# Kernel tuning notes

Hardware: AMD Instinct MI355X
Metric: run time of the kernel (lower is better)

The kernel has to match this reference:

```python
import jax, jax.numpy as jnp
import numpy as np

N_NODES = 50000
N_EDGES = 800000
EMB = 128
NODE_F = 128
EDGE_F = 16
L = 5
BN_EPS = 1e-5


def setup_inputs() -> dict:
    key = jax.random.key(0)
    ks = jax.random.split(key, 12)
    inp = {
        "x": jax.random.normal(ks[0], (N_NODES, NODE_F), jnp.float32),
        "edge_attr": jax.random.normal(ks[1], (N_EDGES, EDGE_F), jnp.float32),
        "edge_index": jax.random.randint(ks[2], (2, N_EDGES), 0, N_NODES, jnp.int32),
        "Wx": jax.random.normal(ks[3], (NODE_F, EMB), jnp.float32) / np.sqrt(NODE_F),
        "bx": jax.random.normal(ks[4], (EMB,), jnp.float32) * 0.01,
        "We": jax.random.normal(ks[5], (L, EDGE_F, EMB), jnp.float32) / np.sqrt(EDGE_F),
        "be": jax.random.normal(ks[6], (L, EMB), jnp.float32) * 0.01,
        "W1": jax.random.normal(ks[7], (L, EMB, 2 * EMB), jnp.float32) / np.sqrt(EMB),
        "b1": jax.random.normal(ks[8], (L, 2 * EMB), jnp.float32) * 0.01,
        "W2": jax.random.normal(ks[9], (L, 2 * EMB, EMB), jnp.float32) / np.sqrt(2 * EMB),
        "b2": jax.random.normal(ks[10], (L, EMB), jnp.float32) * 0.01,
        "gamma": jnp.ones((L, EMB), jnp.float32),
        "beta": jnp.zeros((L, EMB), jnp.float32),
    }
    return inp


def reference(x, edge_attr, edge_index, Wx, bx, We, be, W1, b1, W2, b2, gamma, beta):
    n = x.shape[0]
    num_layers = We.shape[0]
    # add self loops with zero edge attributes (bias of edge_embedding still applies)
    self_idx = jnp.arange(n, dtype=edge_index.dtype)
    src = jnp.concatenate([edge_index[0], self_idx])
    dst = jnp.concatenate([edge_index[1], self_idx])
    ea = jnp.concatenate([edge_attr, jnp.zeros((n, edge_attr.shape[1]), edge_attr.dtype)], axis=0)

    h = x @ Wx + bx  # x_embedding0: [N, EMB]
    for l in range(num_layers):
        eemb = ea @ We[l] + be[l]                     # [E+N, EMB]
        msg = h[src] + eemb                            # gather + add
        agg = jax.ops.segment_sum(msg, dst, num_segments=n)  # scatter-add
        # GIN MLP: emb -> 2*emb -> emb
        h2 = jax.nn.relu(agg @ W1[l] + b1[l]) @ W2[l] + b2[l]
        # BatchNorm1d (training mode: batch statistics, biased variance)
        mean = jnp.mean(h2, axis=0)
        var = jnp.mean((h2 - mean) ** 2, axis=0)
        h2 = (h2 - mean) * jax.lax.rsqrt(var + BN_EPS) * gamma[l] + beta[l]
        if l < num_layers - 1:
            h2 = jax.nn.relu(h2)
        # dropout with drop_ratio=0 is identity
        h = h2
    return h  # JK == 'last'
```

## Files before the change

### kernel.cpp

```cpp
#include <hip/hip_runtime.h>

typedef __bf16 bf16;
typedef __bf16 bf16x2 __attribute__((ext_vector_type(2)));
typedef __bf16 bf16x4 __attribute__((ext_vector_type(4)));
typedef __bf16 bf16x8 __attribute__((ext_vector_type(8)));
typedef float f32x4 __attribute__((ext_vector_type(4)));

#define NN 50000
#define NE 800000
#define EMB 128
#define EDGE_F 16
#define NLAYER 5
#define SCAN_BLOCKS 196

__global__ __launch_bounds__(256) void swz_kernel(
    const float* __restrict__ Wx, const float* __restrict__ W1,
    const float* __restrict__ W2, const float* __restrict__ We,
    bf16* __restrict__ wx_s, bf16* __restrict__ w1_s,
    bf16* __restrict__ w2_s, float* __restrict__ weT)
{
    int t = blockIdx.x * 256 + threadIdx.x;
    if (t < 16384) {
        int k = t >> 7, n = t & 127;
        wx_s[(((k >> 5) << 7) + n) * 32 + (k & 31)] = (bf16)Wx[t];
    } else if (t < 16384 + 163840) {
        int u = t - 16384;
        int l = u / 32768, r = u % 32768;
        int k = r >> 8, n = r & 255;
        w1_s[l * 32768 + (((k >> 5) << 8) + n) * 32 + (k & 31)] = (bf16)W1[u];
    } else if (t < 16384 + 327680) {
        int u = t - (16384 + 163840);
        int l = u / 32768, r = u % 32768;
        int k = r >> 7, n = r & 127;
        w2_s[l * 32768 + (((k >> 5) << 7) + n) * 32 + (k & 31)] = (bf16)W2[u];
    } else if (t < 16384 + 327680 + 10240) {
        int u = t - (16384 + 327680);
        int l = u >> 11, r = u & 2047;
        int c = r >> 4, f = r & 15;
        weT[u] = We[l * 2048 + f * 128 + c];
    }
}

__global__ void count_kernel(const int* __restrict__ dst, int* __restrict__ deg, int nE)
{
    int e = blockIdx.x * 256 + threadIdx.x;
    if (e < nE) atomicAdd(&deg[dst[e]], 1);
}

__global__ __launch_bounds__(256) void deg_bsum_kernel(
    const int* __restrict__ deg, int* __restrict__ bsum, int n)
{
    __shared__ int red[256];
    int i = blockIdx.x * 256 + threadIdx.x;
    red[threadIdx.x] = (i < n) ? deg[i] : 0;
    __syncthreads();
    for (int s = 128; s > 0; s >>= 1) {
        if (threadIdx.x < s) red[threadIdx.x] += red[threadIdx.x + s];
        __syncthreads();
    }
    if (threadIdx.x == 0) bsum[blockIdx.x] = red[0];
}

__global__ __launch_bounds__(256) void bsum_scan_kernel(
    const int* __restrict__ bsum, int* __restrict__ boff,
    int* __restrict__ rowstart, int nb, int n)
{
    __shared__ int v[256];
    int t = threadIdx.x;
    v[t] = (t < nb) ? bsum[t] : 0;
    __syncthreads();
    if (t == 0) {
        int r = 0;
        for (int i = 0; i < nb; ++i) { int x = v[i]; v[i] = r; r += x; }
        rowstart[n] = r;
    }
    __syncthreads();
    if (t < nb) boff[t] = v[t];
}

__global__ __launch_bounds__(256) void chunk_scan_kernel(
    const int* __restrict__ deg, const int* __restrict__ boff,
    int* __restrict__ rowstart, int* __restrict__ cursor, int n)
{
    __shared__ int v[256];
    int t = threadIdx.x;
    int i = blockIdx.x * 256 + t;
    int x = (i < n) ? deg[i] : 0;
    v[t] = x;
    __syncthreads();
    for (int s = 1; s < 256; s <<= 1) {
        int add = (t >= s) ? v[t - s] : 0;
        __syncthreads();
        v[t] += add;
        __syncthreads();
    }
    int ex = v[t] - x + boff[blockIdx.x];
    if (i < n) { rowstart[i] = ex; cursor[i] = ex; }
}

__global__ void fill_kernel(const int* __restrict__ src, const int* __restrict__ dst,
                            int* __restrict__ cursor, int* __restrict__ csr_src,
                            int* __restrict__ csr_e, int nE)
{
    int e = blockIdx.x * 256 + threadIdx.x;
    if (e < nE) {
        int d = dst[e];
        int pos = atomicAdd(&cursor[d], 1);
        csr_src[pos] = src[e];
        csr_e[pos] = e;
    }
}

__global__ __launch_bounds__(256) void ea_gather_kernel(
    const float* __restrict__ edge_attr, const int* __restrict__ rowstart,
    const int* __restrict__ csr_e, float* __restrict__ ea_agg, int n)
{
    int node = blockIdx.x * 16 + (threadIdx.x >> 4);
    int f = threadIdx.x & 15;
    if (node >= n) return;
    int rs = rowstart[node], re = rowstart[node + 1];
    float a = 0.f;
    for (int j = rs; j < re; ++j) {
        int e = csr_e[j];
        a += edge_attr[(size_t)e * EDGE_F + f];
    }
    ea_agg[node * EDGE_F + f] = a;
}

__global__ __launch_bounds__(256) void agg_kernel(
    const bf16* __restrict__ h, const int* __restrict__ rowstart,
    const int* __restrict__ csr_src, const float* __restrict__ ea_agg,
    const float* __restrict__ weT_l, const float* __restrict__ be_l,
    bf16* __restrict__ agg, int n)
{
    int lane = threadIdx.x & 63;
    int node = blockIdx.x * 4 + (threadIdx.x >> 6);
    if (node >= n) return;
    int rs = rowstart[node], re = rowstart[node + 1];
    int c0 = lane * 2;
    float ax = 0.f, ay = 0.f;
    bf16x2 hself = *(const bf16x2*)(h + (size_t)node * EMB + c0);
    int j = rs;
    for (; j + 8 <= re; j += 8) {
        int s0 = csr_src[j], s1 = csr_src[j + 1], s2 = csr_src[j + 2], s3 = csr_src[j + 3];
        int s4 = csr_src[j + 4], s5 = csr_src[j + 5], s6 = csr_src[j + 6], s7 = csr_src[j + 7];
        bf16x2 h0 = *(const bf16x2*)(h + (size_t)s0 * EMB + c0);
        bf16x2 h1 = *(const bf16x2*)(h + (size_t)s1 * EMB + c0);
        bf16x2 h2v = *(const bf16x2*)(h + (size_t)s2 * EMB + c0);
        bf16x2 h3 = *(const bf16x2*)(h + (size_t)s3 * EMB + c0);
        bf16x2 h4 = *(const bf16x2*)(h + (size_t)s4 * EMB + c0);
        bf16x2 h5 = *(const bf16x2*)(h + (size_t)s5 * EMB + c0);
        bf16x2 h6 = *(const bf16x2*)(h + (size_t)s6 * EMB + c0);
        bf16x2 h7 = *(const bf16x2*)(h + (size_t)s7 * EMB + c0);
        ax += (float)h0.x + (float)h1.x + (float)h2v.x + (float)h3.x
            + (float)h4.x + (float)h5.x + (float)h6.x + (float)h7.x;
        ay += (float)h0.y + (float)h1.y + (float)h2v.y + (float)h3.y
            + (float)h4.y + (float)h5.y + (float)h6.y + (float)h7.y;
    }
    for (; j < re; ++j) {
        int s = csr_src[j];
        bf16x2 hv = *(const bf16x2*)(h + (size_t)s * EMB + c0);
        ax += (float)hv.x; ay += (float)hv.y;
    }
    ax += (float)hself.x; ay += (float)hself.y;
    {
        const float* ea = ea_agg + node * EDGE_F;
        const float* w0 = weT_l + (size_t)c0 * 16;
        const float* w1 = weT_l + (size_t)(c0 + 1) * 16;
#pragma unroll
        for (int f = 0; f < 16; ++f) {
            float ef = ea[f];
            ax += ef * w0[f];
            ay += ef * w1[f];
        }
    }
    {
        float dp1 = (float)(re - rs + 1);
        ax += dp1 * be_l[c0];
        ay += dp1 * be_l[c0 + 1];
    }
    bf16x2 o; o.x = (bf16)ax; o.y = (bf16)ay;
    *(bf16x2*)(agg + (size_t)node * EMB + c0) = o;
}

template <int K, int N, bool RELU, bool AFP32, bool STATS>
__global__ __launch_bounds__(256) void gemm_kernel(
    const void* __restrict__ Ap, const bf16* __restrict__ Bswz,
    const float* __restrict__ bias, bf16* __restrict__ outp,
    float* __restrict__ psum, int M)
{
    __shared__ float lstat[STATS ? 1024 : 1];
    if constexpr (STATS) {
        for (int i = threadIdx.x; i < 1024; i += 256) lstat[i] = 0.f;
        __syncthreads();
    }
    const int lane = threadIdx.x & 63;
    const int wave = threadIdx.x >> 6;
    const int m0 = (blockIdx.x * 4 + wave) * 16;
    if (m0 >= M) return;
    const int m = lane & 15, q = lane >> 4;
    constexpr int NF = N / 16, KB = K / 32;

    f32x4 acc[NF];
#pragma unroll
    for (int f = 0; f < NF; ++f) acc[f] = 0.f;

#pragma unroll
    for (int kb = 0; kb < KB; ++kb) {
        bf16x8 a;
        if constexpr (AFP32) {
            const float* ar = (const float*)Ap + (size_t)(m0 + m) * K + kb * 32 + q * 8;
            f32x4 v0 = *(const f32x4*)ar;
            f32x4 v1 = *(const f32x4*)(ar + 4);
#pragma unroll
            for (int j = 0; j < 4; ++j) { a[j] = (bf16)v0[j]; a[4 + j] = (bf16)v1[j]; }
        } else {
            const bf16* ar = (const bf16*)Ap + (size_t)(m0 + m) * K + kb * 32 + q * 8;
            a = *(const bf16x8*)ar;
        }
#pragma unroll
        for (int f = 0; f < NF; ++f) {
            bf16x8 b = *(const bf16x8*)(Bswz + ((size_t)(kb * N + f * 16 + m)) * 32 + q * 8);
            acc[f] = __builtin_amdgcn_mfma_f32_16x16x32_bf16(a, b, acc[f], 0, 0, 0);
        }
    }

#pragma unroll
    for (int f = 0; f < NF; ++f) {
        const int col = f * 16 + m;
        float bv = bias[col];
        float s1 = 0.f, s2 = 0.f;
#pragma unroll
        for (int r = 0; r < 4; ++r) {
            float v = acc[f][r] + bv;
            if (RELU) v = fmaxf(v, 0.f);
            int row = m0 + q * 4 + r;
            outp[(size_t)row * N + col] = (bf16)v;
            if constexpr (STATS) { s1 += v; s2 += v * v; }
        }
        if constexpr (STATS) {
            s1 += __shfl_xor(s1, 16); s1 += __shfl_xor(s1, 32);
            s2 += __shfl_xor(s2, 16); s2 += __shfl_xor(s2, 32);
            if (q == 0) {
                lstat[wave * 128 + col] = s1;
                lstat[512 + wave * 128 + col] = s2;
            }
        }
    }
    if constexpr (STATS) {
        __syncthreads();
        int t = threadIdx.x;
        if (t < 128) {
            float s = lstat[t] + lstat[128 + t] + lstat[256 + t] + lstat[384 + t];
            float ssq = lstat[512 + t] + lstat[640 + t] + lstat[768 + t] + lstat[896 + t];
            psum[(size_t)blockIdx.x * 256 + t] = s;
            psum[(size_t)blockIdx.x * 256 + 128 + t] = ssq;
        }
    }
}

__global__ __launch_bounds__(256) void reduce_stats_kernel(
    const float* __restrict__ psum, float* __restrict__ stats, int nblk)
{
    int c = threadIdx.x;
    float acc = 0.f;
    for (int b = blockIdx.x; b < nblk; b += gridDim.x)
        acc += psum[(size_t)b * 256 + c];
    atomicAdd(&stats[c], acc);
}

__global__ __launch_bounds__(256) void norm_kernel(
    const bf16* __restrict__ h2, const float* __restrict__ sums,
    const float* __restrict__ sumsq, const float* __restrict__ gamma,
    const float* __restrict__ beta, void* __restrict__ outp, int n,
    int relu, int out_fp32)
{
    __shared__ float sc[EMB], sh[EMB];
    int tid = threadIdx.x;
    if (tid < EMB) {
        float inv_n = 1.0f / (float)n;
        float mean = sums[tid] * inv_n;
        float var = sumsq[tid] * inv_n - mean * mean;
        float s = gamma[tid] * rsqrtf(var + 1e-5f);
        sc[tid] = s;
        sh[tid] = beta[tid] - mean * s;
    }
    __syncthreads();
    int total4 = n * (EMB / 4);
    int stride = gridDim.x * blockDim.x;
    for (int i = blockIdx.x * blockDim.x + tid; i < total4; i += stride) {
        bf16x4 hv = ((const bf16x4*)h2)[i];
        int c0 = (i * 4) & (EMB - 1);
        float v0 = (float)hv.x * sc[c0] + sh[c0];
        float v1 = (float)hv.y * sc[c0 + 1] + sh[c0 + 1];
        float v2 = (float)hv.z * sc[c0 + 2] + sh[c0 + 2];
        float v3 = (float)hv.w * sc[c0 + 3] + sh[c0 + 3];
        if (relu) {
            v0 = fmaxf(v0, 0.f); v1 = fmaxf(v1, 0.f);
            v2 = fmaxf(v2, 0.f); v3 = fmaxf(v3, 0.f);
        }
        if (out_fp32) {
            f32x4 o; o.x = v0; o.y = v1; o.z = v2; o.w = v3;
            ((f32x4*)outp)[i] = o;
        } else {
            bf16x4 o;
            o.x = (bf16)v0; o.y = (bf16)v1; o.z = (bf16)v2; o.w = (bf16)v3;
            ((bf16x4*)outp)[i] = o;
        }
    }
}

extern "C" void kernel_launch(void* const* d_in, const int* in_sizes, int n_in,
                              void* d_out, int out_size, void* d_ws, size_t ws_size,
                              hipStream_t stream)
{
    const float* x         = (const float*)d_in[0];
    const float* edge_attr = (const float*)d_in[1];
    const int*   eidx      = (const int*)d_in[2];
    const float* Wx        = (const float*)d_in[3];
    const float* bx        = (const float*)d_in[4];
    const float* We        = (const float*)d_in[5];
    const float* be        = (const float*)d_in[6];
    const float* W1        = (const float*)d_in[7];
    const float* b1        = (const float*)d_in[8];
    const float* W2        = (const float*)d_in[9];
    const float* b2        = (const float*)d_in[10];
    const float* gamma     = (const float*)d_in[11];
    const float* beta      = (const float*)d_in[12];

    size_t off = 0;
    char* base = (char*)d_ws;
    auto alloc = [&](size_t bytes) -> void* {
        void* p = base + off;
        off += (bytes + 255) & ~(size_t)255;
        return p;
    };
    int*   deg      = (int*)alloc(NN * 4);
    float* stats    = (float*)alloc(NLAYER * 256 * 4);
    size_t zero_bytes = off;
    int*   rowstart = (int*)alloc((NN + 1) * 4);
    int*   cursor   = (int*)alloc(NN * 4);
    int*   bsum     = (int*)alloc(SCAN_BLOCKS * 4);
    int*   boff     = (int*)alloc(SCAN_BLOCKS * 4);
    int*   csr_src  = (int*)alloc((size_t)NE * 4);
    int*   csr_e    = (int*)alloc((size_t)NE * 4);
    float* ea_agg   = (float*)alloc((size_t)NN * EDGE_F * 4);
    bf16*  h        = (bf16*)alloc((size_t)NN * EMB * 2);
    bf16*  aggb     = (bf16*)alloc((size_t)NN * EMB * 2);
    bf16*  t1       = (bf16*)alloc((size_t)NN * 2 * EMB * 2);
    bf16*  h2b      = (bf16*)alloc((size_t)NN * EMB * 2);
    float* psum     = (float*)alloc((size_t)782 * 256 * 4);
    bf16*  wx_s     = (bf16*)alloc(16384 * 2);
    bf16*  w1_s     = (bf16*)alloc(163840 * 2);
    bf16*  w2_s     = (bf16*)alloc(163840 * 2);
    float* weT      = (float*)alloc(10240 * 4);
    (void)ws_size; (void)in_sizes; (void)n_in; (void)out_size;

    const int* src = eidx;
    const int* dst = eidx + NE;

    hipMemsetAsync(d_ws, 0, zero_bytes, stream);

    swz_kernel<<<1384, 256, 0, stream>>>(Wx, W1, W2, We, wx_s, w1_s, w2_s, weT);
    count_kernel<<<NE / 256, 256, 0, stream>>>(dst, deg, NE);
    deg_bsum_kernel<<<SCAN_BLOCKS, 256, 0, stream>>>(deg, bsum, NN);
    bsum_scan_kernel<<<1, 256, 0, stream>>>(bsum, boff, rowstart, SCAN_BLOCKS, NN);
    chunk_scan_kernel<<<SCAN_BLOCKS, 256, 0, stream>>>(deg, boff, rowstart, cursor, NN);
    fill_kernel<<<NE / 256, 256, 0, stream>>>(src, dst, cursor, csr_src, csr_e, NE);
    ea_gather_kernel<<<NN / 16, 256, 0, stream>>>(edge_attr, rowstart, csr_e, ea_agg, NN);

    const int gemm_blocks = (NN / 16 + 3) / 4;
    gemm_kernel<128, 128, false, true, false><<<gemm_blocks, 256, 0, stream>>>(
        x, wx_s, bx, h, nullptr, NN);

    for (int l = 0; l < NLAYER; ++l) {
        float* stats_l = stats + l * 256;
        agg_kernel<<<NN / 4, 256, 0, stream>>>(
            h, rowstart, csr_src, ea_agg, weT + l * 2048, be + l * EMB, aggb, NN);
        gemm_kernel<128, 256, true, false, false><<<gemm_blocks, 256, 0, stream>>>(
            aggb, w1_s + l * 32768, b1 + l * 2 * EMB, t1, nullptr, NN);
        gemm_kernel<256, 128, false, false, true><<<gemm_blocks, 256, 0, stream>>>(
            t1, w2_s + l * 32768, b2 + l * EMB, h2b, psum, NN);
        reduce_stats_kernel<<<8, 256, 0, stream>>>(psum, stats_l, gemm_blocks);
        norm_kernel<<<1024, 256, 0, stream>>>(
            h2b, stats_l, stats_l + 128, gamma + l * EMB, beta + l * EMB,
            (l == NLAYER - 1) ? d_out : (void*)h, NN,
            (l < NLAYER - 1) ? 1 : 0, (l == NLAYER - 1) ? 1 : 0);
    }
}
```

Before: 1.030 ms.

## Store node features in column-sliced layout for cache-friendly aggregation gathers

Node features, aggregates and GEMM outputs are stored in 8 column slices of 16 channels ([slice][node][16]). The aggregation kernel processes one slice per block, so each gather touches only a 32-byte row segment and a slice's working set (~1.6 MB) can stay in cache. The edge-embedding term is moved into a separate eaw_kernel that writes a precomputed bf16 tensor each layer. This adds an extra pass over a full N×128 buffer per layer and more kernel launches, and the GEMMs and the norm kernel need index math adapted to the sliced layout.

```diff
diff --git a/kernel.cpp b/kernel.cpp
--- a/kernel.cpp
+++ b/kernel.cpp
@@ -15,9 +15,8 @@
 
 __global__ __launch_bounds__(256) void swz_kernel(
     const float* __restrict__ Wx, const float* __restrict__ W1,
-    const float* __restrict__ W2, const float* __restrict__ We,
-    bf16* __restrict__ wx_s, bf16* __restrict__ w1_s,
-    bf16* __restrict__ w2_s, float* __restrict__ weT)
+    const float* __restrict__ W2,
+    bf16* __restrict__ wx_s, bf16* __restrict__ w1_s, bf16* __restrict__ w2_s)
 {
     int t = blockIdx.x * 256 + threadIdx.x;
     if (t < 16384) {
@@ -33,11 +32,6 @@
         int l = u / 32768, r = u % 32768;
         int k = r >> 7, n = r & 127;
         w2_s[l * 32768 + (((k >> 5) << 7) + n) * 32 + (k & 31)] = (bf16)W2[u];
-    } else if (t < 16384 + 327680 + 10240) {
-        int u = t - (16384 + 327680);
-        int l = u >> 11, r = u & 2047;
-        int c = r >> 4, f = r & 15;
-        weT[u] = We[l * 2048 + f * 128 + c];
     }
 }
 
@@ -127,63 +121,74 @@
     ea_agg[node * EDGE_F + f] = a;
 }
 
+__global__ __launch_bounds__(256) void eaw_kernel(
+    const float* __restrict__ ea_agg, const int* __restrict__ rowstart,
+    const float* __restrict__ We_l, const float* __restrict__ be_l,
+    bf16* __restrict__ eawb, int n)
+{
+    int i = blockIdx.x * 256 + threadIdx.x;
+    int o = i * 2;
+    if (o >= n * EMB) return;
+    int slice = o / (n * 16);
+    int r = o - slice * (n * 16);
+    int node = r >> 4;
+    int c0 = slice * 16 + (r & 15);
+    float dp1 = (float)(rowstart[node + 1] - rowstart[node] + 1);
+    const float* ea = ea_agg + (size_t)node * EDGE_F;
+    float v0 = dp1 * be_l[c0], v1 = dp1 * be_l[c0 + 1];
+#pragma unroll
+    for (int f = 0; f < 16; ++f) {
+        float e = ea[f];
+        v0 += e * We_l[f * EMB + c0];
+        v1 += e * We_l[f * EMB + c0 + 1];
+    }
+    bf16x2 ov; ov.x = (bf16)v0; ov.y = (bf16)v1;
+    *(bf16x2*)(eawb + o) = ov;
+}
+
 __global__ __launch_bounds__(256) void agg_kernel(
-    const bf16* __restrict__ h, const int* __restrict__ rowstart,
-    const int* __restrict__ csr_src, const float* __restrict__ ea_agg,
-    const float* __restrict__ weT_l, const float* __restrict__ be_l,
-    bf16* __restrict__ agg, int n)
-{
-    int lane = threadIdx.x & 63;
-    int node = blockIdx.x * 4 + (threadIdx.x >> 6);
+    const bf16* __restrict__ hsm, const int* __restrict__ rowstart,
+    const int* __restrict__ csr_src, const bf16* __restrict__ eawb,
+    bf16* __restrict__ aggb, int n)
+{
+    const int tid = threadIdx.x;
+    const int slice = blockIdx.x & 7;
+    const int chunk = blockIdx.x >> 3;
+    const int node = chunk * 32 + (tid >> 3);
+    const int ql = tid & 7;
     if (node >= n) return;
-    int rs = rowstart[node], re = rowstart[node + 1];
-    int c0 = lane * 2;
-    float ax = 0.f, ay = 0.f;
-    bf16x2 hself = *(const bf16x2*)(h + (size_t)node * EMB + c0);
+    const size_t sbase = (size_t)slice * n * 16;
+    const bf16* hs = hsm + sbase + ql * 2;
+    const int rs = rowstart[node], re = rowstart[node + 1];
+    float a0 = 0.f, a1 = 0.f;
     int j = rs;
-    for (; j + 8 <= re; j += 8) {
+    for (; j + 4 <= re; j += 4) {
         int s0 = csr_src[j], s1 = csr_src[j + 1], s2 = csr_src[j + 2], s3 = csr_src[j + 3];
-        int s4 = csr_src[j + 4], s5 = csr_src[j + 5], s6 = csr_src[j + 6], s7 = csr_src[j + 7];
-        bf16x2 h0 = *(const bf16x2*)(h + (size_t)s0 * EMB + c0);
-        bf16x2 h1 = *(const bf16x2*)(h + (size_t)s1 * EMB + c0);
-        bf16x2 h2v = *(const bf16x2*)(h + (size_t)s2 * EMB + c0);
-        bf16x2 h3 = *(const bf16x2*)(h + (size_t)s3 * EMB + c0);
-        bf16x2 h4 = *(const bf16x2*)(h + (size_t)s4 * EMB + c0);
-        bf16x2 h5 = *(const bf16x2*)(h + (size_t)s5 * EMB + c0);
-        bf16x2 h6 = *(const bf16x2*)(h + (size_t)s6 * EMB + c0);
-        bf16x2 h7 = *(const bf16x2*)(h + (size_t)s7 * EMB + c0);
-        ax += (float)h0.x + (float)h1.x + (float)h2v.x + (float)h3.x
-            + (float)h4.x + (float)h5.x + (float)h6.x + (float)h7.x;
-        ay += (float)h0.y + (float)h1.y + (float)h2v.y + (float)h3.y
-            + (float)h4.y + (float)h5.y + (float)h6.y + (float)h7.y;
+        bf16x2 r0 = *(const bf16x2*)(hs + (size_t)s0 * 16);
+        bf16x2 r1 = *(const bf16x2*)(hs + (size_t)s1 * 16);
+        bf16x2 r2 = *(const bf16x2*)(hs + (size_t)s2 * 16);
+        bf16x2 r3 = *(const bf16x2*)(hs + (size_t)s3 * 16);
+        a0 += ((float)r0.x + (float)r1.x) + ((float)r2.x + (float)r3.x);
+        a1 += ((float)r0.y + (float)r1.y) + ((float)r2.y + (float)r3.y);
     }
     for (; j < re; ++j) {
         int s = csr_src[j];
-        bf16x2 hv = *(const bf16x2*)(h + (size_t)s * EMB + c0);
-        ax += (float)hv.x; ay += (float)hv.y;
-    }
-    ax += (float)hself.x; ay += (float)hself.y;
+        bf16x2 rv = *(const bf16x2*)(hs + (size_t)s * 16);
+        a0 += (float)rv.x; a1 += (float)rv.y;
+    }
     {
-        const float* ea = ea_agg + node * EDGE_F;
-        const float* w0 = weT_l + (size_t)c0 * 16;
-        const float* w1 = weT_l + (size_t)(c0 + 1) * 16;
-#pragma unroll
-        for (int f = 0; f < 16; ++f) {
-            float ef = ea[f];
-            ax += ef * w0[f];
-            ay += ef * w1[f];
-        }
+        bf16x2 rv = *(const bf16x2*)(hs + (size_t)node * 16);
+        a0 += (float)rv.x; a1 += (float)rv.y;
     }
     {
-        float dp1 = (float)(re - rs + 1);
-        ax += dp1 * be_l[c0];
-        ay += dp1 * be_l[c0 + 1];
-    }
-    bf16x2 o; o.x = (bf16)ax; o.y = (bf16)ay;
-    *(bf16x2*)(agg + (size_t)node * EMB + c0) = o;
-}
-
-template <int K, int N, bool RELU, bool AFP32, bool STATS>
+        bf16x2 ev = *(const bf16x2*)(eawb + sbase + (size_t)node * 16 + ql * 2);
+        a0 += (float)ev.x; a1 += (float)ev.y;
+    }
+    bf16x2 o; o.x = (bf16)a0; o.y = (bf16)a1;
+    *(bf16x2*)(aggb + sbase + (size_t)node * 16 + ql * 2) = o;
+}
+
+template <int K, int N, bool RELU, bool AFP32, bool STATS, bool ASM, bool OSM>
 __global__ __launch_bounds__(256) void gemm_kernel(
     const void* __restrict__ Ap, const bf16* __restrict__ Bswz,
     const float* __restrict__ bias, bf16* __restrict__ outp,
@@ -214,6 +219,10 @@
             f32x4 v1 = *(const f32x4*)(ar + 4);
 #pragma unroll
             for (int j = 0; j < 4; ++j) { a[j] = (bf16)v0[j]; a[4 + j] = (bf16)v1[j]; }
+        } else if constexpr (ASM) {
+            const bf16* ar = (const bf16*)Ap
+                + ((size_t)(kb * 2 + (q >> 1)) * M + (m0 + m)) * 16 + (q & 1) * 8;
+            a = *(const bf16x8*)ar;
         } else {
             const bf16* ar = (const bf16*)Ap + (size_t)(m0 + m) * K + kb * 32 + q * 8;
             a = *(const bf16x8*)ar;
@@ -235,7 +244,10 @@
             float v = acc[f][r] + bv;
             if (RELU) v = fmaxf(v, 0.f);
             int row = m0 + q * 4 + r;
-            outp[(size_t)row * N + col] = (bf16)v;
+            if constexpr (OSM)
+                outp[((size_t)f * M + row) * 16 + m] = (bf16)v;
+            else
+                outp[(size_t)row * N + col] = (bf16)v;
             if constexpr (STATS) { s1 += v; s2 += v * v; }
         }
         if constexpr (STATS) {
@@ -273,7 +285,7 @@
     const bf16* __restrict__ h2, const float* __restrict__ sums,
     const float* __restrict__ sumsq, const float* __restrict__ gamma,
     const float* __restrict__ beta, void* __restrict__ outp, int n,
-    int relu, int out_fp32)
+    int relu, int out_fp32, int sm)
 {
     __shared__ float sc[EMB], sh[EMB];
     int tid = threadIdx.x;
@@ -290,7 +302,14 @@
     int stride = gridDim.x * blockDim.x;
     for (int i = blockIdx.x * blockDim.x + tid; i < total4; i += stride) {
         bf16x4 hv = ((const bf16x4*)h2)[i];
-        int c0 = (i * 4) & (EMB - 1);
+        int c0;
+        if (sm) {
+            int o = i * 4;
+            int slice = o / (n * 16);
+            c0 = slice * 16 + ((o - slice * (n * 16)) & 15);
+        } else {
+            c0 = (i * 4) & (EMB - 1);
+        }
         float v0 = (float)hv.x * sc[c0] + sh[c0];
         float v1 = (float)hv.y * sc[c0 + 1] + sh[c0 + 1];
         float v2 = (float)hv.z * sc[c0 + 2] + sh[c0 + 2];
@@ -347,13 +366,13 @@
     float* ea_agg   = (float*)alloc((size_t)NN * EDGE_F * 4);
     bf16*  h        = (bf16*)alloc((size_t)NN * EMB * 2);
     bf16*  aggb     = (bf16*)alloc((size_t)NN * EMB * 2);
+    bf16*  eawb     = (bf16*)alloc((size_t)NN * EMB * 2);
     bf16*  t1       = (bf16*)alloc((size_t)NN * 2 * EMB * 2);
     bf16*  h2b      = (bf16*)alloc((size_t)NN * EMB * 2);
     float* psum     = (float*)alloc((size_t)782 * 256 * 4);
     bf16*  wx_s     = (bf16*)alloc(16384 * 2);
     bf16*  w1_s     = (bf16*)alloc(163840 * 2);
     bf16*  w2_s     = (bf16*)alloc(163840 * 2);
-    float* weT      = (float*)alloc(10240 * 4);
     (void)ws_size; (void)in_sizes; (void)n_in; (void)out_size;
 
     const int* src = eidx;
@@ -361,7 +380,7 @@
 
     hipMemsetAsync(d_ws, 0, zero_bytes, stream);
 
-    swz_kernel<<<1384, 256, 0, stream>>>(Wx, W1, W2, We, wx_s, w1_s, w2_s, weT);
+    swz_kernel<<<1344, 256, 0, stream>>>(Wx, W1, W2, wx_s, w1_s, w2_s);
     count_kernel<<<NE / 256, 256, 0, stream>>>(dst, deg, NE);
     deg_bsum_kernel<<<SCAN_BLOCKS, 256, 0, stream>>>(deg, bsum, NN);
     bsum_scan_kernel<<<1, 256, 0, stream>>>(bsum, boff, rowstart, SCAN_BLOCKS, NN);
@@ -370,21 +389,29 @@
     ea_gather_kernel<<<NN / 16, 256, 0, stream>>>(edge_attr, rowstart, csr_e, ea_agg, NN);
 
     const int gemm_blocks = (NN / 16 + 3) / 4;
-    gemm_kernel<128, 128, false, true, false><<<gemm_blocks, 256, 0, stream>>>(
+    gemm_kernel<128, 128, false, true, false, false, true><<<gemm_blocks, 256, 0, stream>>>(
         x, wx_s, bx, h, nullptr, NN);
 
+    const int agg_blocks = ((NN + 31) / 32) * 8;
     for (int l = 0; l < NLAYER; ++l) {
         float* stats_l = stats + l * 256;
-        agg_kernel<<<NN / 4, 256, 0, stream>>>(
-            h, rowstart, csr_src, ea_agg, weT + l * 2048, be + l * EMB, aggb, NN);
-        gemm_kernel<128, 256, true, false, false><<<gemm_blocks, 256, 0, stream>>>(
+        eaw_kernel<<<(NN * EMB / 2) / 256, 256, 0, stream>>>(
+            ea_agg, rowstart, We + l * EDGE_F * EMB, be + l * EMB, eawb, NN);
+        agg_kernel<<<agg_blocks, 256, 0, stream>>>(
+            h, rowstart, csr_src, eawb, aggb, NN);
+        gemm_kernel<128, 256, true, false, false, true, false><<<gemm_blocks, 256, 0, stream>>>(
             aggb, w1_s + l * 32768, b1 + l * 2 * EMB, t1, nullptr, NN);
-        gemm_kernel<256, 128, false, false, true><<<gemm_blocks, 256, 0, stream>>>(
-            t1, w2_s + l * 32768, b2 + l * EMB, h2b, psum, NN);
+        if (l < NLAYER - 1)
+            gemm_kernel<256, 128, false, false, true, false, true><<<gemm_blocks, 256, 0, stream>>>(
+                t1, w2_s + l * 32768, b2 + l * EMB, h2b, psum, NN);
+        else
+            gemm_kernel<256, 128, false, false, true, false, false><<<gemm_blocks, 256, 0, stream>>>(
+                t1, w2_s + l * 32768, b2 + l * EMB, h2b, psum, NN);
         reduce_stats_kernel<<<8, 256, 0, stream>>>(psum, stats_l, gemm_blocks);
         norm_kernel<<<1024, 256, 0, stream>>>(
             h2b, stats_l, stats_l + 128, gamma + l * EMB, beta + l * EMB,
             (l == NLAYER - 1) ? d_out : (void*)h, NN,
-            (l < NLAYER - 1) ? 1 : 0, (l == NLAYER - 1) ? 1 : 0);
-    }
-}
+            (l < NLAYER - 1) ? 1 : 0, (l == NLAYER - 1) ? 1 : 0,
+            (l < NLAYER - 1) ? 1 : 0);
+    }
+}
```

Result: slower. 1.058 ms (+2.7%).
